# Kernel optimization log

Hardware: AMD Instinct MI355X
Metric: run time of the kernel (lower is better)

The kernel has to match this reference:

```python
import jax, jax.numpy as jnp
import numpy as np

H = 2          # h_dim (hard-coded in PPIModel)
L = 4          # n_hid rgcn layers
R = 16         # num_rels
B = 8          # num_bases
N = 1_000_000  # num_nodes
E = 16_000_000 # num_edges


def setup_inputs() -> dict:
    key = jax.random.key(0)
    ks = jax.random.split(key, 10)
    features = jax.random.normal(ks[0], (N * H,), dtype=jnp.float32)
    edge_src = jax.random.randint(ks[1], (E,), 0, N)
    edge_dst = jax.random.randint(ks[2], (E,), 0, N)
    edge_type = jax.random.randint(ks[3], (E,), 0, R)
    norm = jax.random.uniform(ks[4], (E, 1), dtype=jnp.float32)
    # Basis-decomposition params per layer: W_r = sum_b comp[r,b] * V[b]
    V = jax.random.normal(ks[5], (L, B, H, H), dtype=jnp.float32) / np.sqrt(H)
    comp = jax.random.normal(ks[6], (L, R, B), dtype=jnp.float32) / np.sqrt(B)
    bias = jnp.zeros((L, H), dtype=jnp.float32)  # DGL RelGraphConv h_bias (default bias=True)
    w_mlp = jax.random.normal(ks[7], (1, N * H), dtype=jnp.float32) / np.sqrt(N * H)
    b_mlp = jnp.zeros((1,), dtype=jnp.float32)
    return dict(features=features, norm=norm, V=V, comp=comp, bias=bias,
                w_mlp=w_mlp, b_mlp=b_mlp,
                edge_src=edge_src, edge_dst=edge_dst, edge_type=edge_type)


def reference(features, norm, V, comp, bias, w_mlp, b_mlp, edge_src, edge_dst, edge_type):
    x = features.reshape(-1, H)          # [N, 2]
    skip = x
    for i in range(L):
        # relation weights from bases: [R, H, H]
        W = jnp.einsum('rb,bio->rio', comp[i], V[i])
        # message per edge: gather src feats, apply relation weight, scale by norm
        msg = jnp.einsum('ei,eio->eo', x[edge_src], W[edge_type]) * norm  # [E, 2]
        # scatter-sum to destination nodes
        h = jax.ops.segment_sum(msg, edge_dst, num_segments=N) + bias[i]  # [N, 2]
        if i < L - 1:
            h = jax.nn.relu(h)
        x = h
        if i % 2 == 1:
            x = x + skip
            skip = x
    flat = x.reshape(1, N * H)           # [1, 2N]
    logit = flat @ w_mlp.T + b_mlp       # [1, 1]
    return jax.nn.sigmoid(logit)
```

## Files before the change

### kernel.cpp

```cpp
#include <hip/hip_runtime.h>
#include <hip/hip_bf16.h>
#include <hip/hip_fp16.h>

#define HD 2
#define LAYERS 4
#define RELS 16
#define BASES 8

#define NB   512
#define BSH  11
#define SBLK 256
#define TPB  256


__global__ void prep_kernel(const float* __restrict__ V, const float* __restrict__ comp,
                            float* __restrict__ W, float* __restrict__ acc) {
    int idx = threadIdx.x;
    if (idx < LAYERS * RELS * 4) {
        int l  = idx >> 6;
        int r  = (idx >> 2) & (RELS - 1);
        int io = idx & 3;
        float s = 0.f;
        for (int b = 0; b < BASES; ++b)
            s += comp[(l * RELS + r) * BASES + b] * V[(l * BASES + b) * 4 + io];
        W[idx] = s;
    }
    if (idx == 0) *acc = 0.f;
}

__global__ void finalize_kernel(const float* __restrict__ acc,
                                const float* __restrict__ b_mlp,
                                float* __restrict__ out) {
    float v = *acc + b_mlp[0];
    out[0] = 1.f / (1.f + expf(-v));
}

__global__ __launch_bounds__(TPB) void f2h_kernel(const float2* __restrict__ in,
                                                  __half2* __restrict__ out, int N) {
    int i = blockIdx.x * blockDim.x + threadIdx.x;
    if (i < N) out[i] = __float22half2_rn(in[i]);
}


__global__ __launch_bounds__(TPB) void hist_kernel(const int* __restrict__ dst,
                                                   unsigned* __restrict__ blockhist,
                                                   int E, int per) {
    __shared__ unsigned hist[NB];
    for (int i = threadIdx.x; i < NB; i += TPB) hist[i] = 0u;
    __syncthreads();
    int blk = blockIdx.x;
    int e0 = blk * per;
    int e1 = min(e0 + per, E);
    const int4* dst4 = (const int4*)dst;
    int g0 = e0 >> 2, g1 = e1 >> 2;
    for (int g = g0 + threadIdx.x; g < g1; g += TPB) {
        int4 d = dst4[g];
        atomicAdd(&hist[((unsigned)d.x) >> BSH], 1u);
        atomicAdd(&hist[((unsigned)d.y) >> BSH], 1u);
        atomicAdd(&hist[((unsigned)d.z) >> BSH], 1u);
        atomicAdd(&hist[((unsigned)d.w) >> BSH], 1u);
    }
    for (int e = (g1 << 2) + threadIdx.x; e < e1; e += TPB)
        atomicAdd(&hist[((unsigned)dst[e]) >> BSH], 1u);
    __syncthreads();
    for (int i = threadIdx.x; i < NB; i += TPB)
        blockhist[(size_t)blk * NB + i] = hist[i];
}

__global__ __launch_bounds__(TPB) void colscan_kernel(unsigned* __restrict__ blockhist,
                                                      unsigned* __restrict__ totals) {
    int bucket = blockIdx.x;
    int t = threadIdx.x;
    unsigned v = blockhist[(size_t)t * NB + bucket];
    __shared__ unsigned s[TPB];
    s[t] = v;
    __syncthreads();
    for (int off = 1; off < TPB; off <<= 1) {
        unsigned x = (t >= off) ? s[t - off] : 0u;
        __syncthreads();
        s[t] += x;
        __syncthreads();
    }
    blockhist[(size_t)t * NB + bucket] = s[t] - v;
    if (t == TPB - 1) totals[bucket] = s[TPB - 1];
}

__global__ __launch_bounds__(TPB) void scan_kernel(const unsigned* __restrict__ totals,
                                                   unsigned* __restrict__ base) {
    int t = threadIdx.x;
    unsigned v0 = totals[2 * t];
    unsigned v1 = totals[2 * t + 1];
    unsigned run = v0 + v1;
    __shared__ unsigned s[TPB];
    s[t] = run;
    __syncthreads();
    for (int off = 1; off < TPB; off <<= 1) {
        unsigned x = (t >= off) ? s[t - off] : 0u;
        __syncthreads();
        s[t] += x;
        __syncthreads();
    }
    unsigned b0 = s[t] - run;
    base[2 * t]     = b0;
    base[2 * t + 1] = b0 + v0;
    if (t == TPB - 1) base[NB] = s[TPB - 1];
}

__global__ __launch_bounds__(TPB) void scatter_kernel(const int* __restrict__ src,
                                                      const int* __restrict__ dst,
                                                      const int* __restrict__ typ,
                                                      const float* __restrict__ norm,
                                                      const unsigned* __restrict__ blockhist,
                                                      const unsigned* __restrict__ base,
                                                      unsigned long long* __restrict__ packed,
                                                      int E, int per) {
    __shared__ unsigned cnt[NB];
    int blk = blockIdx.x;
    for (int i = threadIdx.x; i < NB; i += TPB)
        cnt[i] = blockhist[(size_t)blk * NB + i] + base[i];
    __syncthreads();
    int e0 = blk * per;
    int e1 = min(e0 + per, E);
    const int4*   src4 = (const int4*)src;
    const int4*   dst4 = (const int4*)dst;
    const int4*   typ4 = (const int4*)typ;
    const float4* nrm4 = (const float4*)norm;
    int g0 = e0 >> 2, g1 = e1 >> 2;

#define PUT(SS, DD, TT, NN)                                                       \
    {                                                                             \
        unsigned _d = (unsigned)(DD);                                             \
        unsigned _bucket = _d >> BSH;                                             \
        unsigned _pos = atomicAdd(&cnt[_bucket], 1u);                             \
        unsigned _w1 = (_d & ((1u << BSH) - 1u)) | (((unsigned)(TT)) << 12) |     \
                       ((unsigned)__half_as_ushort(__float2half_rn(NN)) << 16);   \
        packed[_pos] = (unsigned long long)(unsigned)(SS) |                       \
                       ((unsigned long long)_w1 << 32);                           \
    }

    for (int g = g0 + threadIdx.x; g < g1; g += TPB) {
        int4 s = src4[g];
        int4 d = dst4[g];
        int4 t = typ4[g];
        float4 nm = nrm4[g];
        PUT(s.x, d.x, t.x, nm.x)
        PUT(s.y, d.y, t.y, nm.y)
        PUT(s.z, d.z, t.z, nm.z)
        PUT(s.w, d.w, t.w, nm.w)
    }
    for (int e = (g1 << 2) + threadIdx.x; e < e1; e += TPB)
        PUT(src[e], dst[e], typ[e], norm[e])
#undef PUT
}

__global__ __launch_bounds__(TPB) void bucket_edge_kernel(
    const unsigned long long* __restrict__ packed,
    const unsigned* __restrict__ base,
    const __half2* __restrict__ xh,
    const float* __restrict__ Wl,
    const float* __restrict__ bias2,
    const float2* __restrict__ skipF,
    const __half2* __restrict__ skipH,
    __half2* __restrict__ outH,
    const float2* __restrict__ w2,
    float* __restrict__ acc,
    int N, int do_relu)
{
    __shared__ float acc0[1 << BSH];
    __shared__ float acc1[1 << BSH];
    __shared__ float sW[64];
    __shared__ float wred[4];

    int t = threadIdx.x;
#pragma unroll
    for (int k = 0; k < (1 << BSH) / TPB; ++k) {
        acc0[k * TPB + t] = 0.f;
        acc1[k * TPB + t] = 0.f;
    }
    if (t < 64) sW[t] = Wl[t];
    __syncthreads();

    int b  = blockIdx.x;
    int e0 = (int)base[b];
    int e1 = (int)base[b + 1];

    for (int e = e0 + t; e < e1; e += 2 * TPB) {
        unsigned long long p0 = __builtin_nontemporal_load(&packed[e]);
        int e2 = e + TPB;
        bool has2 = e2 < e1;
        unsigned long long p1 = has2 ? __builtin_nontemporal_load(&packed[e2]) : 0ull;

        float2 xv0 = __half22float2(xh[(unsigned)p0]);
        float2 xv1 = has2 ? __half22float2(xh[(unsigned)p1]) : make_float2(0.f, 0.f);

        {
            unsigned w1  = (unsigned)(p0 >> 32);
            unsigned dof = w1 & ((1u << BSH) - 1u);
            int wb = (int)((w1 >> 12) & 15u) << 2;
            float nm = __half2float(__ushort_as_half((unsigned short)(w1 >> 16)));
            float m0 = (xv0.x * sW[wb + 0] + xv0.y * sW[wb + 2]) * nm;
            float m1 = (xv0.x * sW[wb + 1] + xv0.y * sW[wb + 3]) * nm;
            atomicAdd(&acc0[dof], m0);
            atomicAdd(&acc1[dof], m1);
        }
        if (has2) {
            unsigned w1  = (unsigned)(p1 >> 32);
            unsigned dof = w1 & ((1u << BSH) - 1u);
            int wb = (int)((w1 >> 12) & 15u) << 2;
            float nm = __half2float(__ushort_as_half((unsigned short)(w1 >> 16)));
            float m0 = (xv1.x * sW[wb + 0] + xv1.y * sW[wb + 2]) * nm;
            float m1 = (xv1.x * sW[wb + 1] + xv1.y * sW[wb + 3]) * nm;
            atomicAdd(&acc0[dof], m0);
            atomicAdd(&acc1[dof], m1);
        }
    }
    __syncthreads();

    float b0 = bias2[0], b1 = bias2[1];
    int nodeBase = b << BSH;
    float part = 0.f;
#pragma unroll
    for (int k = 0; k < (1 << BSH) / TPB; ++k) {
        int i = k * TPB + t;
        int node = nodeBase + i;
        if (node < N) {
            float v0 = acc0[i] + b0;
            float v1 = acc1[i] + b1;
            if (do_relu) { v0 = fmaxf(v0, 0.f); v1 = fmaxf(v1, 0.f); }
            if (skipF) { float2 sv = skipF[node]; v0 += sv.x; v1 += sv.y; }
            if (skipH) { float2 sv = __half22float2(skipH[node]); v0 += sv.x; v1 += sv.y; }
            if (outH)  outH[node] = __floats2half2_rn(v0, v1);
            if (w2)    { float2 wv = w2[node]; part += v0 * wv.x + v1 * wv.y; }
        }
    }
    if (w2) {
        for (int off = 32; off > 0; off >>= 1) part += __shfl_down(part, off, 64);
        int lane = t & 63, wv = t >> 6;
        if (lane == 0) wred[wv] = part;
        __syncthreads();
        if (t == 0) atomicAdd(acc, wred[0] + wred[1] + wred[2] + wred[3]);
    }
}


__global__ void zero_kernel(float4* __restrict__ p, int n4) {
    int i = blockIdx.x * blockDim.x + threadIdx.x;
    int stride = gridDim.x * blockDim.x;
    for (; i < n4; i += stride) p[i] = make_float4(0.f, 0.f, 0.f, 0.f);
}

__global__ __launch_bounds__(256) void edge_kernel(
    const float* __restrict__ x, const int* __restrict__ src,
    const int* __restrict__ dst, const int* __restrict__ typ,
    const float* __restrict__ norm, const float* __restrict__ Wl,
    float* __restrict__ h, int E)
{
    __shared__ float sW[64];
    if (threadIdx.x < 64) sW[threadIdx.x] = Wl[threadIdx.x];
    __syncthreads();
    const float2* __restrict__ x2 = (const float2*)x;
    int tid = blockIdx.x * blockDim.x + threadIdx.x;
    int stride = gridDim.x * blockDim.x;
    for (int e = tid; e < E; e += stride) {
        int s = src[e], d = dst[e], t = typ[e];
        float nm = norm[e];
        float2 xv = x2[s];
        int wb = t << 2;
        float m0 = (xv.x * sW[wb + 0] + xv.y * sW[wb + 2]) * nm;
        float m1 = (xv.x * sW[wb + 1] + xv.y * sW[wb + 3]) * nm;
        atomicAdd(&h[2 * (size_t)d],     m0);
        atomicAdd(&h[2 * (size_t)d + 1], m1);
    }
}

__global__ void node_kernel(const float* __restrict__ h, const float* __restrict__ bias_l,
                            const float* __restrict__ skip, float* __restrict__ xout,
                            int N, int do_relu)
{
    float b0 = bias_l[0], b1 = bias_l[1];
    const float2* __restrict__ h2 = (const float2*)h;
    const float2* __restrict__ s2 = (const float2*)skip;
    float2* __restrict__ o2 = (float2*)xout;
    int i = blockIdx.x * blockDim.x + threadIdx.x;
    int stride = gridDim.x * blockDim.x;
    for (; i < N; i += stride) {
        float2 v = h2[i];
        v.x += b0; v.y += b1;
        if (do_relu) { v.x = fmaxf(v.x, 0.f); v.y = fmaxf(v.y, 0.f); }
        if (skip) { float2 sv = s2[i]; v.x += sv.x; v.y += sv.y; }
        o2[i] = v;
    }
}

__global__ __launch_bounds__(256) void dot_kernel(const float* __restrict__ a,
                                                  const float* __restrict__ b,
                                                  float* __restrict__ acc, int n)
{
    int i = blockIdx.x * blockDim.x + threadIdx.x;
    int stride = gridDim.x * blockDim.x;
    float s = 0.f;
    int n4 = n >> 2;
    const float4* __restrict__ a4 = (const float4*)a;
    const float4* __restrict__ b4 = (const float4*)b;
    for (int g = i; g < n4; g += stride) {
        float4 av = a4[g], bv = b4[g];
        s += av.x * bv.x + av.y * bv.y + av.z * bv.z + av.w * bv.w;
    }
    for (int e = (n4 << 2) + i; e < n; e += stride) s += a[e] * b[e];
    for (int off = 32; off > 0; off >>= 1) s += __shfl_down(s, off, 64);
    __shared__ float wsum[4];
    int lane = threadIdx.x & 63, wv = threadIdx.x >> 6;
    if (lane == 0) wsum[wv] = s;
    __syncthreads();
    if (threadIdx.x == 0) atomicAdd(acc, wsum[0] + wsum[1] + wsum[2] + wsum[3]);
}


static inline size_t align256(size_t x) { return (x + 255) & ~(size_t)255; }

extern "C" void kernel_launch(void* const* d_in, const int* in_sizes, int n_in,
                              void* d_out, int out_size, void* d_ws, size_t ws_size,
                              hipStream_t stream) {
    const float* features = (const float*)d_in[0];
    const float* norm     = (const float*)d_in[1];
    const float* V        = (const float*)d_in[2];
    const float* comp     = (const float*)d_in[3];
    const float* bias     = (const float*)d_in[4];
    const float* w_mlp    = (const float*)d_in[5];
    const float* b_mlp    = (const float*)d_in[6];
    const int*   esrc     = (const int*)d_in[7];
    const int*   edst     = (const int*)d_in[8];
    const int*   etyp     = (const int*)d_in[9];

    int NH = in_sizes[0];
    int N  = NH / 2;
    int E  = in_sizes[7];

    char* ws = (char*)d_ws;
    size_t oA    = 0;
    size_t oB    = align256(oA + (size_t)NH * 4);
    size_t oC    = align256(oB + (size_t)NH * 4);
    size_t oW    = align256(oC + (size_t)NH * 4);
    size_t oAcc  = align256(oW + 1024);
    size_t oBase = align256(oAcc + 4);
    size_t oTot  = align256(oBase + (size_t)(NB + 1) * 4);
    size_t oHist = align256(oTot + (size_t)NB * 4);
    size_t oFh   = align256(oHist + (size_t)SBLK * NB * 4);
    size_t oAh   = align256(oFh + (size_t)N * 4);
    size_t oBh   = align256(oAh + (size_t)N * 4);
    size_t oCh   = align256(oBh + (size_t)N * 4);
    size_t oPack = align256(oCh + (size_t)N * 4);
    size_t REQ   = oPack + (size_t)E * 8;

    float* A   = (float*)(ws + oA);
    float* B   = (float*)(ws + oB);
    float* C   = (float*)(ws + oC);
    float* W   = (float*)(ws + oW);
    float* acc = (float*)(ws + oAcc);

    prep_kernel<<<1, 256, 0, stream>>>(V, comp, W, acc);

    if (ws_size >= REQ && N <= (1 << 20)) {
        unsigned* base      = (unsigned*)(ws + oBase);
        unsigned* totals    = (unsigned*)(ws + oTot);
        unsigned* blockhist = (unsigned*)(ws + oHist);
        __half2*  Fh        = (__half2*)(ws + oFh);
        __half2*  Ah        = (__half2*)(ws + oAh);
        __half2*  Bh        = (__half2*)(ws + oBh);
        __half2*  Ch        = (__half2*)(ws + oCh);
        unsigned long long* packed = (unsigned long long*)(ws + oPack);

        int per = (((E + SBLK - 1) / SBLK) + 3) & ~3;

        f2h_kernel    <<<(N + TPB - 1) / TPB, TPB, 0, stream>>>((const float2*)features, Fh, N);
        hist_kernel   <<<SBLK, TPB, 0, stream>>>(edst, blockhist, E, per);
        colscan_kernel<<<NB,   TPB, 0, stream>>>(blockhist, totals);
        scan_kernel   <<<1,    TPB, 0, stream>>>(totals, base);
        scatter_kernel<<<SBLK, TPB, 0, stream>>>(esrc, edst, etyp, norm,
                                                 blockhist, base, packed, E, per);

        int nbkt = (N + (1 << BSH) - 1) >> BSH;
        const float2* feat2 = (const float2*)features;
        const float2* w2    = (const float2*)w_mlp;

        bucket_edge_kernel<<<nbkt, TPB, 0, stream>>>(packed, base, Fh, W + 0,
            bias + 0, nullptr, nullptr, Ah, nullptr, acc, N, 1);
        bucket_edge_kernel<<<nbkt, TPB, 0, stream>>>(packed, base, Ah, W + 64,
            bias + 2, feat2, nullptr, Bh, nullptr, acc, N, 1);
        bucket_edge_kernel<<<nbkt, TPB, 0, stream>>>(packed, base, Bh, W + 128,
            bias + 4, nullptr, nullptr, Ch, nullptr, acc, N, 1);
        bucket_edge_kernel<<<nbkt, TPB, 0, stream>>>(packed, base, Ch, W + 192,
            bias + 6, nullptr, Bh, nullptr, w2, acc, N, 0);
    } else {
        int zb = (NH / 4 + 255) / 256;
        int eb = (E / 4 + 255) / 256;
        int nb = (N + 255) / 256;
        int db = (NH / 4 + 255) / 256;

        zero_kernel<<<zb, 256, 0, stream>>>((float4*)A, NH / 4);
        edge_kernel<<<eb, 256, 0, stream>>>(features, esrc, edst, etyp, norm, W + 0, A, E);
        node_kernel<<<nb, 256, 0, stream>>>(A, bias + 0, nullptr, A, N, 1);

        zero_kernel<<<zb, 256, 0, stream>>>((float4*)B, NH / 4);
        edge_kernel<<<eb, 256, 0, stream>>>(A, esrc, edst, etyp, norm, W + 64, B, E);
        node_kernel<<<nb, 256, 0, stream>>>(B, bias + 2, features, B, N, 1);

        zero_kernel<<<zb, 256, 0, stream>>>((float4*)C, NH / 4);
        edge_kernel<<<eb, 256, 0, stream>>>(B, esrc, edst, etyp, norm, W + 128, C, E);
        node_kernel<<<nb, 256, 0, stream>>>(C, bias + 4, nullptr, C, N, 1);

        zero_kernel<<<zb, 256, 0, stream>>>((float4*)A, NH / 4);
        edge_kernel<<<eb, 256, 0, stream>>>(C, esrc, edst, etyp, norm, W + 192, A, E);
        node_kernel<<<nb, 256, 0, stream>>>(A, bias + 6, B, A, N, 0);

        dot_kernel<<<db, 256, 0, stream>>>(A, w_mlp, acc, NH);
    }

    finalize_kernel<<<1, 1, 0, stream>>>(acc, b_mlp, (float*)d_out);
}
```

Before: 1.198 ms.

## Split each destination bucket's edges across three blocks with partial-sum reduction

Each layer's bucketed edge pass now runs on a 2D grid, giving every node bucket SPLIT=3 blocks. Each block accumulates its share of the bucket's edges in shared memory and writes a partial result per node to a separate slice of the float workspace. A new per-node kernel sums the slices and applies bias, ReLU, skip connection, the half-precision store and the final dot product. The aim is more blocks in flight, since about 489 buckets leave the GPU underfilled. The edge loop is also unrolled to four loads per thread, and the histogram and scatter phases double SBLK to 512 with a two-element column scan. The cost is writing and re-reading three float partials per node each layer plus an extra launch per layer, and it assumes the A..C workspace holds three strides.

```diff
diff --git a/kernel.cpp b/kernel.cpp
--- a/kernel.cpp
+++ b/kernel.cpp
@@ -7,10 +7,11 @@
 #define RELS 16
 #define BASES 8
 
-#define NB   512
-#define BSH  11
-#define SBLK 256
-#define TPB  256
+#define NB    512
+#define BSH   11
+#define SBLK  512
+#define TPB   256
+#define SPLIT 3
 
 
 __global__ void prep_kernel(const float* __restrict__ V, const float* __restrict__ comp,
@@ -71,9 +72,11 @@
                                                       unsigned* __restrict__ totals) {
     int bucket = blockIdx.x;
     int t = threadIdx.x;
-    unsigned v = blockhist[(size_t)t * NB + bucket];
+    unsigned v0 = blockhist[(size_t)(2 * t)     * NB + bucket];
+    unsigned v1 = blockhist[(size_t)(2 * t + 1) * NB + bucket];
+    unsigned run = v0 + v1;
     __shared__ unsigned s[TPB];
-    s[t] = v;
+    s[t] = run;
     __syncthreads();
     for (int off = 1; off < TPB; off <<= 1) {
         unsigned x = (t >= off) ? s[t - off] : 0u;
@@ -81,7 +84,9 @@
         s[t] += x;
         __syncthreads();
     }
-    blockhist[(size_t)t * NB + bucket] = s[t] - v;
+    unsigned base = s[t] - run;
+    blockhist[(size_t)(2 * t)     * NB + bucket] = base;
+    blockhist[(size_t)(2 * t + 1) * NB + bucket] = base + v0;
     if (t == TPB - 1) totals[bucket] = s[TPB - 1];
 }
 
@@ -153,11 +158,84 @@
 #undef PUT
 }
 
-__global__ __launch_bounds__(TPB) void bucket_edge_kernel(
+__global__ __launch_bounds__(TPB) void edge_split_kernel(
     const unsigned long long* __restrict__ packed,
     const unsigned* __restrict__ base,
     const __half2* __restrict__ xh,
     const float* __restrict__ Wl,
+    float* __restrict__ Pbase,
+    long long pstride,
+    int N)
+{
+    __shared__ float acc0[1 << BSH];
+    __shared__ float acc1[1 << BSH];
+    __shared__ float sW[64];
+
+    int t = threadIdx.x;
+#pragma unroll
+    for (int k = 0; k < (1 << BSH) / TPB; ++k) {
+        acc0[k * TPB + t] = 0.f;
+        acc1[k * TPB + t] = 0.f;
+    }
+    if (t < 64) sW[t] = Wl[t];
+    __syncthreads();
+
+    int b = blockIdx.x;
+    int s = blockIdx.y;
+    int e0 = (int)base[b];
+    int len = (int)base[b + 1] - e0;
+    int es = e0 + (int)((long long)len * s / SPLIT);
+    int ee = e0 + (int)((long long)len * (s + 1) / SPLIT);
+
+    for (int e = es + t; e < ee; e += 4 * TPB) {
+        int eA = e, eB = e + TPB, eC = e + 2 * TPB, eD = e + 3 * TPB;
+        bool hB = eB < ee, hC = eC < ee, hD = eD < ee;
+        unsigned long long p0 = __builtin_nontemporal_load(&packed[eA]);
+        unsigned long long p1 = hB ? __builtin_nontemporal_load(&packed[eB]) : 0ull;
+        unsigned long long p2 = hC ? __builtin_nontemporal_load(&packed[eC]) : 0ull;
+        unsigned long long p3 = hD ? __builtin_nontemporal_load(&packed[eD]) : 0ull;
+
+        float2 x0 = __half22float2(xh[(unsigned)p0]);
+        float2 x1 = hB ? __half22float2(xh[(unsigned)p1]) : make_float2(0.f, 0.f);
+        float2 x2 = hC ? __half22float2(xh[(unsigned)p2]) : make_float2(0.f, 0.f);
+        float2 x3 = hD ? __half22float2(xh[(unsigned)p3]) : make_float2(0.f, 0.f);
+
+#define DO_EDGE(PP, XV)                                                        \
+        {                                                                      \
+            unsigned _w1  = (unsigned)((PP) >> 32);                            \
+            unsigned _dof = _w1 & ((1u << BSH) - 1u);                          \
+            int _wb = (int)((_w1 >> 12) & 15u) << 2;                           \
+            float _nm = __half2float(__ushort_as_half((unsigned short)(_w1 >> 16))); \
+            float _m0 = ((XV).x * sW[_wb + 0] + (XV).y * sW[_wb + 2]) * _nm;   \
+            float _m1 = ((XV).x * sW[_wb + 1] + (XV).y * sW[_wb + 3]) * _nm;   \
+            atomicAdd(&acc0[_dof], _m0);                                       \
+            atomicAdd(&acc1[_dof], _m1);                                       \
+        }
+        DO_EDGE(p0, x0)
+        if (hB) DO_EDGE(p1, x1)
+        if (hC) DO_EDGE(p2, x2)
+        if (hD) DO_EDGE(p3, x3)
+#undef DO_EDGE
+    }
+    __syncthreads();
+
+    float* P = Pbase + (size_t)s * (size_t)pstride;
+    int nodeBase = b << BSH;
+#pragma unroll
+    for (int k = 0; k < (1 << BSH) / TPB; ++k) {
+        int i = k * TPB + t;
+        int node = nodeBase + i;
+        if (node < N) {
+            unsigned long long uv =
+                ((unsigned long long)__float_as_uint(acc1[i]) << 32) |
+                (unsigned long long)__float_as_uint(acc0[i]);
+            __builtin_nontemporal_store(uv, (unsigned long long*)(P + 2 * (size_t)node));
+        }
+    }
+}
+
+__global__ __launch_bounds__(TPB) void node_sum_kernel(
+    const float* __restrict__ Pbase, long long pstride,
     const float* __restrict__ bias2,
     const float2* __restrict__ skipF,
     const __half2* __restrict__ skipH,
@@ -166,79 +244,30 @@
     float* __restrict__ acc,
     int N, int do_relu)
 {
-    __shared__ float acc0[1 << BSH];
-    __shared__ float acc1[1 << BSH];
-    __shared__ float sW[64];
     __shared__ float wred[4];
-
-    int t = threadIdx.x;
+    int i = blockIdx.x * TPB + threadIdx.x;
+    float part = 0.f;
+    if (i < N) {
+        float v0 = 0.f, v1 = 0.f;
 #pragma unroll
-    for (int k = 0; k < (1 << BSH) / TPB; ++k) {
-        acc0[k * TPB + t] = 0.f;
-        acc1[k * TPB + t] = 0.f;
-    }
-    if (t < 64) sW[t] = Wl[t];
-    __syncthreads();
-
-    int b  = blockIdx.x;
-    int e0 = (int)base[b];
-    int e1 = (int)base[b + 1];
-
-    for (int e = e0 + t; e < e1; e += 2 * TPB) {
-        unsigned long long p0 = __builtin_nontemporal_load(&packed[e]);
-        int e2 = e + TPB;
-        bool has2 = e2 < e1;
-        unsigned long long p1 = has2 ? __builtin_nontemporal_load(&packed[e2]) : 0ull;
-
-        float2 xv0 = __half22float2(xh[(unsigned)p0]);
-        float2 xv1 = has2 ? __half22float2(xh[(unsigned)p1]) : make_float2(0.f, 0.f);
-
-        {
-            unsigned w1  = (unsigned)(p0 >> 32);
-            unsigned dof = w1 & ((1u << BSH) - 1u);
-            int wb = (int)((w1 >> 12) & 15u) << 2;
-            float nm = __half2float(__ushort_as_half((unsigned short)(w1 >> 16)));
-            float m0 = (xv0.x * sW[wb + 0] + xv0.y * sW[wb + 2]) * nm;
-            float m1 = (xv0.x * sW[wb + 1] + xv0.y * sW[wb + 3]) * nm;
-            atomicAdd(&acc0[dof], m0);
-            atomicAdd(&acc1[dof], m1);
+        for (int s = 0; s < SPLIT; ++s) {
+            const float2* Ps = (const float2*)(Pbase + (size_t)s * (size_t)pstride);
+            float2 pv = Ps[i];
+            v0 += pv.x; v1 += pv.y;
         }
-        if (has2) {
-            unsigned w1  = (unsigned)(p1 >> 32);
-            unsigned dof = w1 & ((1u << BSH) - 1u);
-            int wb = (int)((w1 >> 12) & 15u) << 2;
-            float nm = __half2float(__ushort_as_half((unsigned short)(w1 >> 16)));
-            float m0 = (xv1.x * sW[wb + 0] + xv1.y * sW[wb + 2]) * nm;
-            float m1 = (xv1.x * sW[wb + 1] + xv1.y * sW[wb + 3]) * nm;
-            atomicAdd(&acc0[dof], m0);
-            atomicAdd(&acc1[dof], m1);
-        }
-    }
-    __syncthreads();
-
-    float b0 = bias2[0], b1 = bias2[1];
-    int nodeBase = b << BSH;
-    float part = 0.f;
-#pragma unroll
-    for (int k = 0; k < (1 << BSH) / TPB; ++k) {
-        int i = k * TPB + t;
-        int node = nodeBase + i;
-        if (node < N) {
-            float v0 = acc0[i] + b0;
-            float v1 = acc1[i] + b1;
-            if (do_relu) { v0 = fmaxf(v0, 0.f); v1 = fmaxf(v1, 0.f); }
-            if (skipF) { float2 sv = skipF[node]; v0 += sv.x; v1 += sv.y; }
-            if (skipH) { float2 sv = __half22float2(skipH[node]); v0 += sv.x; v1 += sv.y; }
-            if (outH)  outH[node] = __floats2half2_rn(v0, v1);
-            if (w2)    { float2 wv = w2[node]; part += v0 * wv.x + v1 * wv.y; }
-        }
+        v0 += bias2[0]; v1 += bias2[1];
+        if (do_relu) { v0 = fmaxf(v0, 0.f); v1 = fmaxf(v1, 0.f); }
+        if (skipF) { float2 sv = skipF[i]; v0 += sv.x; v1 += sv.y; }
+        if (skipH) { float2 sv = __half22float2(skipH[i]); v0 += sv.x; v1 += sv.y; }
+        if (outH)  outH[i] = __floats2half2_rn(v0, v1);
+        if (w2)    { float2 wv = w2[i]; part = v0 * wv.x + v1 * wv.y; }
     }
     if (w2) {
         for (int off = 32; off > 0; off >>= 1) part += __shfl_down(part, off, 64);
-        int lane = t & 63, wv = t >> 6;
+        int lane = threadIdx.x & 63, wv = threadIdx.x >> 6;
         if (lane == 0) wred[wv] = part;
         __syncthreads();
-        if (t == 0) atomicAdd(acc, wred[0] + wred[1] + wred[2] + wred[3]);
+        if (threadIdx.x == 0) atomicAdd(acc, wred[0] + wred[1] + wred[2] + wred[3]);
     }
 }
 
@@ -370,6 +399,8 @@
         __half2*  Ch        = (__half2*)(ws + oCh);
         unsigned long long* packed = (unsigned long long*)(ws + oPack);
 
+        long long pstride = (long long)((oB - oA) / 4);
+
         int per = (((E + SBLK - 1) / SBLK) + 3) & ~3;
 
         f2h_kernel    <<<(N + TPB - 1) / TPB, TPB, 0, stream>>>((const float2*)features, Fh, N);
@@ -380,17 +411,23 @@
                                                  blockhist, base, packed, E, per);
 
         int nbkt = (N + (1 << BSH) - 1) >> BSH;
+        dim3 egrid(nbkt, SPLIT);
+        int nnb = (N + TPB - 1) / TPB;
         const float2* feat2 = (const float2*)features;
         const float2* w2    = (const float2*)w_mlp;
 
-        bucket_edge_kernel<<<nbkt, TPB, 0, stream>>>(packed, base, Fh, W + 0,
-            bias + 0, nullptr, nullptr, Ah, nullptr, acc, N, 1);
-        bucket_edge_kernel<<<nbkt, TPB, 0, stream>>>(packed, base, Ah, W + 64,
-            bias + 2, feat2, nullptr, Bh, nullptr, acc, N, 1);
-        bucket_edge_kernel<<<nbkt, TPB, 0, stream>>>(packed, base, Bh, W + 128,
-            bias + 4, nullptr, nullptr, Ch, nullptr, acc, N, 1);
-        bucket_edge_kernel<<<nbkt, TPB, 0, stream>>>(packed, base, Ch, W + 192,
-            bias + 6, nullptr, Bh, nullptr, w2, acc, N, 0);
+        edge_split_kernel<<<egrid, TPB, 0, stream>>>(packed, base, Fh, W + 0, A, pstride, N);
+        node_sum_kernel  <<<nnb,   TPB, 0, stream>>>(A, pstride, bias + 0,
+            nullptr, nullptr, Ah, nullptr, acc, N, 1);
+        edge_split_kernel<<<egrid, TPB, 0, stream>>>(packed, base, Ah, W + 64, A, pstride, N);
+        node_sum_kernel  <<<nnb,   TPB, 0, stream>>>(A, pstride, bias + 2,
+            feat2, nullptr, Bh, nullptr, acc, N, 1);
+        edge_split_kernel<<<egrid, TPB, 0, stream>>>(packed, base, Bh, W + 128, A, pstride, N);
+        node_sum_kernel  <<<nnb,   TPB, 0, stream>>>(A, pstride, bias + 4,
+            nullptr, nullptr, Ch, nullptr, acc, N, 1);
+        edge_split_kernel<<<egrid, TPB, 0, stream>>>(packed, base, Ch, W + 192, A, pstride, N);
+        node_sum_kernel  <<<nnb,   TPB, 0, stream>>>(A, pstride, bias + 6,
+            nullptr, Bh, nullptr, w2, acc, N, 0);
     } else {
         int zb = (NH / 4 + 255) / 256;
         int eb = (E / 4 + 255) / 256;
```

After: 1.215 ms. Within noise of the previous version (+1.5%).
